# Kernel optimization log

Measured on AMD Instinct MI355X. Metric: run time of the kernel, lower is better.

## Reference

```python
import math
import jax, jax.numpy as jnp
import numpy as np

T, B, C, H = 1024, 4, 1024, 16
D = C // H  # d_k = 64


def setup_inputs() -> dict:
    key = jax.random.key(0)
    ks = jax.random.split(key, 16)
    s = 0.02
    return {
        "query": jax.random.normal(ks[0], (T, B, C), jnp.float32),
        "key": jax.random.normal(ks[1], (T, B, C), jnp.float32),
        "value": jax.random.normal(ks[2], (T, B, C), jnp.float32),
        "pos_emb": jax.random.normal(ks[3], (2 * T - 1, 1, C), jnp.float32),
        "Wq": jax.random.normal(ks[4], (C, C), jnp.float32) * s,
        "bq": jnp.zeros((C,), jnp.float32),
        "Wk": jax.random.normal(ks[5], (C, C), jnp.float32) * s,
        "bk": jnp.zeros((C,), jnp.float32),
        "Wv": jax.random.normal(ks[6], (C, C), jnp.float32) * s,
        "bv": jnp.zeros((C,), jnp.float32),
        "Wp": jax.random.normal(ks[7], (C, C), jnp.float32) * s,
        "Wo": jax.random.normal(ks[8], (C, C), jnp.float32) * s,
        "bo": jnp.zeros((C,), jnp.float32),
        "pos_bias_u": jax.random.normal(ks[9], (H, D), jnp.float32) * s,
        "pos_bias_v": jax.random.normal(ks[10], (H, D), jnp.float32) * s,
    }


def rel_shift(x):
    # x: [B, H, T, P] with P = 2T-1 -> [B, H, T, T]
    b, h, t, p = x.shape
    x = jnp.pad(x, ((0, 0), (0, 0), (0, 0), (1, 0)))  # [B,H,T,P+1]
    x = x.reshape(b, h, p + 1, t)[:, :, 1:, :].reshape(b, h, t, p)
    return x[..., : p // 2 + 1]


def reference(query, key, value, pos_emb, Wq, bq, Wk, bk, Wv, bv, Wp, Wo, bo,
              pos_bias_u, pos_bias_v):
    # T x B x C -> B x T x C
    q_in = query.transpose(1, 0, 2)
    k_in = key.transpose(1, 0, 2)
    v_in = value.transpose(1, 0, 2)
    p_in = pos_emb.transpose(1, 0, 2)  # [1, 2T-1, C]

    q = (q_in @ Wq.T + bq).reshape(B, T, H, D)            # [B,T,H,D]
    k = (k_in @ Wk.T + bk).reshape(B, T, H, D)
    v = (v_in @ Wv.T + bv).reshape(B, T, H, D)
    p = (p_in @ Wp.T).reshape(2 * T - 1, H, D)            # [2T-1,H,D]

    # content (ac) and position (bd) scores
    matrix_ac = jnp.einsum('bthd,bshd->bhts', q + pos_bias_u, k)   # [B,H,T,T]
    matrix_bd = jnp.einsum('bthd,phd->bhtp', q + pos_bias_v, p)    # [B,H,T,2T-1]
    matrix_bd = rel_shift(matrix_bd)                               # [B,H,T,T]

    scores = (matrix_ac + matrix_bd) / math.sqrt(D)
    scores = jnp.clip(scores, -1e8, 1e8)
    attn = jax.nn.softmax(scores.astype(jnp.float32), axis=-1).astype(scores.dtype)

    x = jnp.einsum('bhts,bshd->bthd', attn, v).reshape(B, T, C)
    out = x @ Wo.T + bo
    return out.transpose(1, 0, 2)  # T x B x C
```

## Files before the change

kernel.cpp:

```cpp
#include <hip/hip_runtime.h>
#include <hip/hip_bf16.h>
#include <math.h>

#define T_SEQ 1024
#define NB 4
#define NH 16
#define DD 64
#define CC 1024

typedef __attribute__((ext_vector_type(8))) short short8;
typedef __attribute__((ext_vector_type(4))) float floatx4;
typedef __attribute__((ext_vector_type(4))) unsigned short ushort4v;

#define MFMA(a, b, c) __builtin_amdgcn_mfma_f32_16x16x32_bf16((a), (b), (c), 0, 0, 0)

__device__ inline float bf2f(unsigned short u) {
  union { unsigned int i; float f; } c; c.i = ((unsigned int)u) << 16; return c.f;
}
__device__ inline unsigned short f2bf(float x) {
  union { float f; unsigned int i; } c; c.f = x;
  unsigned int u = c.i;
  u += 0x7fff + ((u >> 16) & 1);
  return (unsigned short)(u >> 16);
}

__device__ __forceinline__ void gload_lds16(const void* g, void* l) {
  __builtin_amdgcn_global_load_lds(
      (const __attribute__((address_space(1))) unsigned int*)g,
      (__attribute__((address_space(3))) unsigned int*)l, 16, 0, 0);
}

__global__ __launch_bounds__(256) void convert_kernel(
    const float* __restrict__ q, const float* __restrict__ k,
    const float* __restrict__ v, const float* __restrict__ pe_in,
    const float* __restrict__ wq, const float* __restrict__ wk,
    const float* __restrict__ wv, const float* __restrict__ wp,
    const float* __restrict__ wo,
    unsigned short* __restrict__ qo, unsigned short* __restrict__ ko,
    unsigned short* __restrict__ vo, unsigned short* __restrict__ po,
    unsigned short* __restrict__ wqo, unsigned short* __restrict__ wko,
    unsigned short* __restrict__ wvo, unsigned short* __restrict__ wpo,
    unsigned short* __restrict__ woo)
{
  const int i = blockIdx.x * 256 + threadIdx.x;
  const float* src; unsigned short* dst; int off;
  if      (i < 524288)  { src = q;     dst = qo;  off = i; }
  else if (i < 1048576) { src = k;     dst = ko;  off = i - 524288; }
  else if (i < 1572864) { src = v;     dst = vo;  off = i - 1048576; }
  else if (i < 1834880) { src = pe_in; dst = po;  off = i - 1572864; }
  else if (i < 1965952) { src = wq;    dst = wqo; off = i - 1834880; }
  else if (i < 2097024) { src = wk;    dst = wko; off = i - 1965952; }
  else if (i < 2228096) { src = wv;    dst = wvo; off = i - 2097024; }
  else if (i < 2359168) { src = wp;    dst = wpo; off = i - 2228096; }
  else if (i < 2490240) { src = wo;    dst = woo; off = i - 2359168; }
  else {
    const int j = i - 2490240;
    *(short8*)&po[2047 * 1024 + j * 8] = (short8){0, 0, 0, 0, 0, 0, 0, 0};
    return;
  }
  const float4 a0 = *(const float4*)(src + (size_t)off * 8);
  const float4 a1 = *(const float4*)(src + (size_t)off * 8 + 4);
  short8 val = (short8){(short)f2bf(a0.x), (short)f2bf(a0.y), (short)f2bf(a0.z), (short)f2bf(a0.w),
                        (short)f2bf(a1.x), (short)f2bf(a1.y), (short)f2bf(a1.z), (short)f2bf(a1.w)};
  *(short8*)&dst[(size_t)off * 8] = val;
}

template <int OUT_BF16>
__device__ __forceinline__ void gemm_core(
    const unsigned short* __restrict__ A, const unsigned short* __restrict__ Wt,
    const float* __restrict__ bias, void* __restrict__ Cv,
    unsigned short* As, unsigned short* Bs, int N, int K, int bm, int bn)
{
  const int tid = threadIdx.x;
  const int lane = tid & 63;
  const int w = tid >> 6;
  const int l15 = lane & 15, quad = lane >> 4;
  const int rw = (w >> 1) * 64, cw = (w & 1) * 64;

  floatx4 acc[4][4];
#pragma unroll
  for (int i = 0; i < 4; ++i)
#pragma unroll
    for (int j = 0; j < 4; ++j) acc[i][j] = (floatx4){0.f, 0.f, 0.f, 0.f};

  const int lrow = lane >> 2, lcol = (lane & 3) * 8;
  const unsigned short* Ag = A + (size_t)(bm + w * 32 + lrow) * K + lcol;
  const unsigned short* Wg = Wt + (size_t)(bn + w * 32 + lrow) * K + lcol;
  unsigned short* AsW = As + w * 1024;
  unsigned short* BsW = Bs + w * 1024;

  for (int k0 = 0; k0 < K; k0 += 32) {
    gload_lds16(Ag + k0, AsW);
    gload_lds16(Ag + 16 * K + k0, AsW + 512);
    gload_lds16(Wg + k0, BsW);
    gload_lds16(Wg + 16 * K + k0, BsW + 512);
    __syncthreads();

    short8 af[4], bfr[4];
#pragma unroll
    for (int i = 0; i < 4; ++i)
      af[i] = *(short8*)&As[(rw + i * 16 + l15) * 32 + quad * 8];
#pragma unroll
    for (int j = 0; j < 4; ++j)
      bfr[j] = *(short8*)&Bs[(cw + j * 16 + l15) * 32 + quad * 8];
#pragma unroll
    for (int i = 0; i < 4; ++i)
#pragma unroll
      for (int j = 0; j < 4; ++j)
        acc[i][j] = MFMA(af[i], bfr[j], acc[i][j]);
    __syncthreads();
  }

#pragma unroll
  for (int j = 0; j < 4; ++j) {
    const int col = bn + cw + j * 16 + l15;
    const float bj = bias ? bias[col] : 0.f;
#pragma unroll
    for (int i = 0; i < 4; ++i) {
      const int row0 = bm + rw + i * 16 + quad * 4;
#pragma unroll
      for (int reg = 0; reg < 4; ++reg) {
        const float v = acc[i][j][reg] + bj;
        if (OUT_BF16)
          ((unsigned short*)Cv)[(size_t)(row0 + reg) * N + col] = f2bf(v);
        else
          ((float*)Cv)[(size_t)(row0 + reg) * N + col] = v;
      }
    }
  }
}

struct GemmJob { const unsigned short* A; const unsigned short* Wt;
                 const float* bias; unsigned short* C; int mtiles; };
struct GemmJobs { GemmJob j[3]; };

__global__ __launch_bounds__(256) void gemm_qkp(GemmJobs jobs) {
  __shared__ __align__(16) unsigned short As[128 * 32];
  __shared__ __align__(16) unsigned short Bs[128 * 32];
  GemmJob jb = jobs.j[blockIdx.z];
  if ((int)blockIdx.y >= jb.mtiles) return;
  gemm_core<1>(jb.A, jb.Wt, jb.bias, jb.C, As, Bs, 1024, 1024,
               blockIdx.y * 128, blockIdx.x * 128);
}

template <int OUT_BF16>
__global__ __launch_bounds__(256) void gemm_one(
    const unsigned short* __restrict__ A, const unsigned short* __restrict__ Wt,
    const float* __restrict__ bias, void* __restrict__ Cv) {
  __shared__ __align__(16) unsigned short As[128 * 32];
  __shared__ __align__(16) unsigned short Bs[128 * 32];
  gemm_core<OUT_BF16>(A, Wt, bias, Cv, As, Bs, 1024, 1024,
                      blockIdx.y * 128, blockIdx.x * 128);
}

__global__ __launch_bounds__(256) void transpose_v(
    const unsigned short* __restrict__ vb, unsigned short* __restrict__ vT)
{
  __shared__ __align__(16) unsigned short Lt[64 * 136];
  const int t0 = blockIdx.x * 128;
  const int h = blockIdx.y, b = blockIdx.z;
  const int tid = threadIdx.x;

#pragma unroll
  for (int cc = 0; cc < 4; ++cc) {
    const int idx = tid + cc * 256;
    const int r = idx >> 3, pc = idx & 7;
    short8 val = *(const short8*)(vb + ((size_t)((t0 + r) * 4 + b)) * 1024 + h * 64 + pc * 8);
#pragma unroll
    for (int e = 0; e < 8; ++e)
      Lt[(pc * 8 + e) * 136 + r] = (unsigned short)val[e];
  }
  __syncthreads();
#pragma unroll
  for (int cc = 0; cc < 4; ++cc) {
    const int idx = tid + cc * 256;
    const int d = idx >> 4, tc = idx & 15;
    short8 v2 = *(short8*)&Lt[d * 136 + tc * 8];
    *(short8*)(vT + ((size_t)((b * 16 + h) * 64 + d)) * 1024 + t0 + tc * 8) = v2;
  }
}

__global__ __launch_bounds__(256) void precompute_kernel(
    const unsigned short* __restrict__ kb, const unsigned short* __restrict__ pb,
    const float* __restrict__ pbu, const float* __restrict__ pbv,
    float* __restrict__ uk, float* __restrict__ vp)
{
  const int i = blockIdx.x * 256 + threadIdx.x;
  if (i < 65536) {
    const int b = i >> 14, h = (i >> 10) & 15, s = i & 1023;
    const unsigned short* kr = kb + ((size_t)(s * 4 + b)) * 1024 + h * 64;
    const float* ur = pbu + h * 64;
    float sum = 0.f;
#pragma unroll
    for (int c = 0; c < 8; ++c) {
      short8 kv = *(const short8*)(kr + c * 8);
#pragma unroll
      for (int e = 0; e < 8; ++e) sum += bf2f((unsigned short)kv[e]) * ur[c * 8 + e];
    }
    uk[i] = sum;
  } else if (i < 98304) {
    const int j = i - 65536;
    const int idx = j >> 4, h = j & 15;
    const unsigned short* pr = pb + (size_t)idx * 1024 + h * 64;
    const float* vr = pbv + h * 64;
    float sum = 0.f;
#pragma unroll
    for (int c = 0; c < 8; ++c) {
      short8 pv = *(const short8*)(pr + c * 8);
#pragma unroll
      for (int e = 0; e < 8; ++e) sum += bf2f((unsigned short)pv[e]) * vr[c * 8 + e];
    }
    vp[(idx << 4) + h] = sum;
  }
}

__global__ __launch_bounds__(256) void attn_kernel(
    const unsigned short* __restrict__ qb, const unsigned short* __restrict__ kb,
    const unsigned short* __restrict__ pb, const unsigned short* __restrict__ vT,
    const float* __restrict__ uk, const float* __restrict__ vp,
    unsigned short* __restrict__ xb)
{
  __shared__ __align__(16) unsigned short Pb[64 * 136];
  __shared__ __align__(16) float BDf[64 * 196];
  __shared__ float uk_s[128], vp_w[192];
  __shared__ float pmax[2][64], psum[2][64];
  __shared__ float m_row[64], l_row[64], alpha_row[64];

  const int tid = threadIdx.x;
  const int lane = tid & 63;
  const int w = tid >> 6;
  const int l15 = lane & 15, quad = lane >> 4;
  const int th = w & 1, sh = w >> 1;

  const int flat = blockIdx.x + (blockIdx.y << 4) + (blockIdx.z << 8);
  const int x8 = flat & 7, s8 = flat >> 3;
  const int hb = x8 * 8 + (s8 >> 4);
  const int t0 = (s8 & 15) * 64;
  const int b = hb >> 4, h = hb & 15;

  short8 qf[2][2];
#pragma unroll
  for (int tt = 0; tt < 2; ++tt)
#pragma unroll
    for (int kk = 0; kk < 2; ++kk) {
      const int t = t0 + th * 32 + tt * 16 + l15;
      qf[tt][kk] = *(const short8*)(qb + ((size_t)(t * 4 + b)) * 1024 + h * 64 + kk * 32 + quad * 8);
    }

  floatx4 of[2][2];
#pragma unroll
  for (int i = 0; i < 2; ++i)
#pragma unroll
    for (int j = 0; j < 2; ++j) of[i][j] = (floatx4){0.f, 0.f, 0.f, 0.f};

  if (tid < 64) { m_row[tid] = -3.0e38f; l_row[tid] = 0.f; }
  __syncthreads();

  for (int s0 = 0; s0 < 1024; s0 += 128) {
    const int w0 = s0 - t0 + 960;

    if (tid < 128) uk_s[tid] = uk[((b * 16 + h) << 10) + s0 + tid];
    if (tid < 192) vp_w[tid] = vp[(((size_t)(w0 + tid)) << 4) + h];

    {
      floatx4 bd[6][2];
#pragma unroll
      for (int jt = 0; jt < 6; ++jt) {
        const int jj = sh * 96 + jt * 16 + l15;
        const unsigned short* pr = pb + ((size_t)(w0 + jj)) * 1024 + h * 64;
        short8 pf0 = *(const short8*)(pr + quad * 8);
        short8 pf1 = *(const short8*)(pr + 32 + quad * 8);
#pragma unroll
        for (int tt = 0; tt < 2; ++tt) {
          floatx4 z = (floatx4){0.f, 0.f, 0.f, 0.f};
          z = MFMA(pf0, qf[tt][0], z);
          z = MFMA(pf1, qf[tt][1], z);
          bd[jt][tt] = z;
        }
      }
#pragma unroll
      for (int jt = 0; jt < 6; ++jt)
#pragma unroll
        for (int tt = 0; tt < 2; ++tt) {
          const int tloc = th * 32 + tt * 16 + l15;
          const int jjb = sh * 96 + jt * 16 + quad * 4;
          *(float4*)&BDf[tloc * 196 + jjb] =
              make_float4(bd[jt][tt][0], bd[jt][tt][1], bd[jt][tt][2], bd[jt][tt][3]);
        }
    }

    floatx4 st[4][2];
#pragma unroll
    for (int stile = 0; stile < 4; ++stile) {
      const int srow = s0 + sh * 64 + stile * 16 + l15;
      const unsigned short* kr = kb + ((size_t)(srow * 4 + b)) * 1024 + h * 64;
      short8 kf0 = *(const short8*)(kr + quad * 8);
      short8 kf1 = *(const short8*)(kr + 32 + quad * 8);
#pragma unroll
      for (int tt = 0; tt < 2; ++tt) {
        floatx4 z = (floatx4){0.f, 0.f, 0.f, 0.f};
        z = MFMA(kf0, qf[tt][0], z);
        z = MFMA(kf1, qf[tt][1], z);
        st[stile][tt] = z;
      }
    }
    __syncthreads();

    float lmax[2] = {-3.0e38f, -3.0e38f};
#pragma unroll
    for (int stile = 0; stile < 4; ++stile)
#pragma unroll
      for (int tt = 0; tt < 2; ++tt) {
        const int tloc = th * 32 + tt * 16 + l15;
#pragma unroll
        for (int reg = 0; reg < 4; ++reg) {
          const int sloc = sh * 64 + stile * 16 + quad * 4 + reg;
          const int jj = sloc - tloc + 63;
          float v = 0.125f * (st[stile][tt][reg] + BDf[tloc * 196 + jj] +
                              uk_s[sloc] + vp_w[jj]);
          st[stile][tt][reg] = v;
          lmax[tt] = fmaxf(lmax[tt], v);
        }
      }
#pragma unroll
    for (int tt = 0; tt < 2; ++tt) {
      lmax[tt] = fmaxf(lmax[tt], __shfl_xor(lmax[tt], 16));
      lmax[tt] = fmaxf(lmax[tt], __shfl_xor(lmax[tt], 32));
    }
    if (quad == 0) {
      pmax[sh][th * 32 + l15] = lmax[0];
      pmax[sh][th * 32 + 16 + l15] = lmax[1];
    }
    __syncthreads();

    if (tid < 64) {
      const float mo = m_row[tid];
      const float mn = fmaxf(mo, fmaxf(pmax[0][tid], pmax[1][tid]));
      alpha_row[tid] = __expf(mo - mn);
      m_row[tid] = mn;
    }
    __syncthreads();

    float lsum[2] = {0.f, 0.f};
    float mt[2];
#pragma unroll
    for (int tt = 0; tt < 2; ++tt) mt[tt] = m_row[th * 32 + tt * 16 + l15];
#pragma unroll
    for (int stile = 0; stile < 4; ++stile)
#pragma unroll
      for (int tt = 0; tt < 2; ++tt) {
        float p0 = __expf(st[stile][tt][0] - mt[tt]);
        float p1 = __expf(st[stile][tt][1] - mt[tt]);
        float p2 = __expf(st[stile][tt][2] - mt[tt]);
        float p3 = __expf(st[stile][tt][3] - mt[tt]);
        lsum[tt] += p0 + p1 + p2 + p3;
        const int tloc = th * 32 + tt * 16 + l15;
        const int sb = sh * 64 + stile * 16 + quad * 4;
        ushort4v pk = (ushort4v){f2bf(p0), f2bf(p1), f2bf(p2), f2bf(p3)};
        *(ushort4v*)&Pb[tloc * 136 + sb] = pk;
      }
#pragma unroll
    for (int tt = 0; tt < 2; ++tt) {
      lsum[tt] += __shfl_xor(lsum[tt], 16);
      lsum[tt] += __shfl_xor(lsum[tt], 32);
    }
    if (quad == 0) {
      psum[sh][th * 32 + l15] = lsum[0];
      psum[sh][th * 32 + 16 + l15] = lsum[1];
    }
#pragma unroll
    for (int tt = 0; tt < 2; ++tt)
#pragma unroll
      for (int reg = 0; reg < 4; ++reg) {
        const float ar = alpha_row[th * 32 + tt * 16 + quad * 4 + reg];
        of[tt][0][reg] *= ar;
        of[tt][1][reg] *= ar;
      }
    __syncthreads();

    if (tid < 64)
      l_row[tid] = l_row[tid] * alpha_row[tid] + psum[0][tid] + psum[1][tid];
#pragma unroll
    for (int kk2 = 0; kk2 < 4; ++kk2) {
      short8 pa[2], vf[2];
#pragma unroll
      for (int tt = 0; tt < 2; ++tt)
        pa[tt] = *(short8*)&Pb[(th * 32 + tt * 16 + l15) * 136 + kk2 * 32 + quad * 8];
#pragma unroll
      for (int dt = 0; dt < 2; ++dt)
        vf[dt] = *(const short8*)(vT + ((size_t)((b * 16 + h) * 64 + sh * 32 + dt * 16 + l15)) * 1024 +
                                  s0 + kk2 * 32 + quad * 8);
#pragma unroll
      for (int tt = 0; tt < 2; ++tt)
#pragma unroll
        for (int dt = 0; dt < 2; ++dt)
          of[tt][dt] = MFMA(pa[tt], vf[dt], of[tt][dt]);
    }
  }
  __syncthreads();

#pragma unroll
  for (int tt = 0; tt < 2; ++tt)
#pragma unroll
    for (int reg = 0; reg < 4; ++reg) {
      const int t = th * 32 + tt * 16 + quad * 4 + reg;
      const float il = 1.f / l_row[t];
#pragma unroll
      for (int dt = 0; dt < 2; ++dt) {
        const int d = sh * 32 + dt * 16 + l15;
        xb[((size_t)((t0 + t) * 4 + b)) * 1024 + h * 64 + d] = f2bf(of[tt][dt][reg] * il);
      }
    }
}

extern "C" void kernel_launch(void* const* d_in, const int* in_sizes, int n_in,
                              void* d_out, int out_size, void* d_ws, size_t ws_size,
                              hipStream_t stream) {
  const float* query   = (const float*)d_in[0];
  const float* key_    = (const float*)d_in[1];
  const float* value   = (const float*)d_in[2];
  const float* pos_emb = (const float*)d_in[3];
  const float* Wq  = (const float*)d_in[4];
  const float* bq  = (const float*)d_in[5];
  const float* Wk  = (const float*)d_in[6];
  const float* bk  = (const float*)d_in[7];
  const float* Wv  = (const float*)d_in[8];
  const float* bv  = (const float*)d_in[9];
  const float* Wp  = (const float*)d_in[10];
  const float* Wo  = (const float*)d_in[11];
  const float* bo  = (const float*)d_in[12];
  const float* pbu = (const float*)d_in[13];
  const float* pbv = (const float*)d_in[14];
  float* out = (float*)d_out;

  unsigned short* U = (unsigned short*)d_ws;
  unsigned short* qin = U;
  unsigned short* kin = U + 4194304;
  unsigned short* vin = U + 8388608;
  unsigned short* pe  = U + 12582912;
  unsigned short* wq  = U + 14680064;
  unsigned short* wk  = U + 15728640;
  unsigned short* wv  = U + 16777216;
  unsigned short* wp  = U + 17825792;
  unsigned short* wo  = U + 18874368;
  unsigned short* qb  = U + 19922944;
  unsigned short* kb  = U + 24117248;
  unsigned short* pb  = U + 28311552;
  unsigned short* vTb = U + 30408704;
  unsigned short* vpo = kin;
  unsigned short* xb  = qin;
  float* fbase = (float*)(U + 34603008);
  float* uk = fbase;
  float* vp = fbase + 65536;

  const dim3 blk(256);

  convert_kernel<<<dim3(9728), blk, 0, stream>>>(
      query, key_, value, pos_emb, Wq, Wk, Wv, Wp, Wo,
      qin, kin, vin, pe, wq, wk, wv, wp, wo);

  GemmJobs jobs;
  jobs.j[0] = GemmJob{qin, wq, bq, qb, 32};
  jobs.j[1] = GemmJob{kin, wk, bk, kb, 32};
  jobs.j[2] = GemmJob{pe,  wp, nullptr, pb, 16};
  gemm_qkp<<<dim3(8, 32, 3), blk, 0, stream>>>(jobs);

  gemm_one<1><<<dim3(8, 32), blk, 0, stream>>>(vin, wv, bv, vpo);

  transpose_v<<<dim3(8, 16, 4), blk, 0, stream>>>(vpo, vTb);

  precompute_kernel<<<dim3(384), blk, 0, stream>>>(kb, pb, pbu, pbv, uk, vp);

  attn_kernel<<<dim3(16, 16, 4), blk, 0, stream>>>(qb, kb, pb, vTb, uk, vp, xb);

  gemm_one<0><<<dim3(8, 32), blk, 0, stream>>>(xb, wo, bo, out);
}
```

Before: 352.8 us.

## Merge V GEMM into batched projection launch and slim attention kernel LDS/sync

Folds the V projection GEMM into the batched Q/K/P GEMM launch, saving one kernel launch and giving the GPU a larger grid. In the attention kernel the BD and P tiles now share one LDS buffer, and the running max and sum move from shared memory into registers. This removes per-iteration barriers and lets the launch bound request three blocks per CU. V fragments are also loaded at the top of each tile to hide latency. The costs are higher register pressure and aliasing the vT buffer onto the pe workspace, which must not be live when the transpose writes it.

```diff
diff --git a/kernel.cpp b/kernel.cpp
--- a/kernel.cpp
+++ b/kernel.cpp
@@ -132,9 +132,9 @@
 
 struct GemmJob { const unsigned short* A; const unsigned short* Wt;
                  const float* bias; unsigned short* C; int mtiles; };
-struct GemmJobs { GemmJob j[3]; };
-
-__global__ __launch_bounds__(256) void gemm_qkp(GemmJobs jobs) {
+struct GemmJobs { GemmJob j[4]; };
+
+__global__ __launch_bounds__(256) void gemm_qkvp(GemmJobs jobs) {
   __shared__ __align__(16) unsigned short As[128 * 32];
   __shared__ __align__(16) unsigned short Bs[128 * 32];
   GemmJob jb = jobs.j[blockIdx.z];
@@ -214,17 +214,18 @@
   }
 }
 
-__global__ __launch_bounds__(256) void attn_kernel(
+__global__ __launch_bounds__(256, 3) void attn_kernel(
     const unsigned short* __restrict__ qb, const unsigned short* __restrict__ kb,
     const unsigned short* __restrict__ pb, const unsigned short* __restrict__ vT,
     const float* __restrict__ uk, const float* __restrict__ vp,
     unsigned short* __restrict__ xb)
 {
-  __shared__ __align__(16) unsigned short Pb[64 * 136];
-  __shared__ __align__(16) float BDf[64 * 196];
+  __shared__ __align__(16) unsigned char SU[64 * 196 * 4];
+  float* BDf = (float*)SU;
+  unsigned short* Pb = (unsigned short*)SU;
   __shared__ float uk_s[128], vp_w[192];
   __shared__ float pmax[2][64], psum[2][64];
-  __shared__ float m_row[64], l_row[64], alpha_row[64];
+  __shared__ float alpha_s[64];
 
   const int tid = threadIdx.x;
   const int lane = tid & 63;
@@ -253,40 +254,38 @@
 #pragma unroll
     for (int j = 0; j < 2; ++j) of[i][j] = (floatx4){0.f, 0.f, 0.f, 0.f};
 
-  if (tid < 64) { m_row[tid] = -3.0e38f; l_row[tid] = 0.f; }
-  __syncthreads();
+  float m_reg[2] = {-3.0e38f, -3.0e38f};
+  float l_reg[2][4] = {{0.f, 0.f, 0.f, 0.f}, {0.f, 0.f, 0.f, 0.f}};
 
   for (int s0 = 0; s0 < 1024; s0 += 128) {
     const int w0 = s0 - t0 + 960;
 
+    short8 vf[4][2];
+#pragma unroll
+    for (int kk2 = 0; kk2 < 4; ++kk2)
+#pragma unroll
+      for (int dt = 0; dt < 2; ++dt)
+        vf[kk2][dt] = *(const short8*)(vT + ((size_t)((b * 16 + h) * 64 + sh * 32 + dt * 16 + l15)) * 1024 +
+                                       s0 + kk2 * 32 + quad * 8);
+
     if (tid < 128) uk_s[tid] = uk[((b * 16 + h) << 10) + s0 + tid];
     if (tid < 192) vp_w[tid] = vp[(((size_t)(w0 + tid)) << 4) + h];
 
-    {
-      floatx4 bd[6][2];
-#pragma unroll
-      for (int jt = 0; jt < 6; ++jt) {
-        const int jj = sh * 96 + jt * 16 + l15;
-        const unsigned short* pr = pb + ((size_t)(w0 + jj)) * 1024 + h * 64;
-        short8 pf0 = *(const short8*)(pr + quad * 8);
-        short8 pf1 = *(const short8*)(pr + 32 + quad * 8);
-#pragma unroll
-        for (int tt = 0; tt < 2; ++tt) {
-          floatx4 z = (floatx4){0.f, 0.f, 0.f, 0.f};
-          z = MFMA(pf0, qf[tt][0], z);
-          z = MFMA(pf1, qf[tt][1], z);
-          bd[jt][tt] = z;
-        }
-      }
-#pragma unroll
-      for (int jt = 0; jt < 6; ++jt)
-#pragma unroll
-        for (int tt = 0; tt < 2; ++tt) {
-          const int tloc = th * 32 + tt * 16 + l15;
-          const int jjb = sh * 96 + jt * 16 + quad * 4;
-          *(float4*)&BDf[tloc * 196 + jjb] =
-              make_float4(bd[jt][tt][0], bd[jt][tt][1], bd[jt][tt][2], bd[jt][tt][3]);
-        }
+#pragma unroll
+    for (int jt = 0; jt < 6; ++jt) {
+      const int jj = sh * 96 + jt * 16 + l15;
+      const unsigned short* pr = pb + ((size_t)(w0 + jj)) * 1024 + h * 64;
+      short8 pf0 = *(const short8*)(pr + quad * 8);
+      short8 pf1 = *(const short8*)(pr + 32 + quad * 8);
+#pragma unroll
+      for (int tt = 0; tt < 2; ++tt) {
+        floatx4 z = (floatx4){0.f, 0.f, 0.f, 0.f};
+        z = MFMA(pf0, qf[tt][0], z);
+        z = MFMA(pf1, qf[tt][1], z);
+        const int tloc = th * 32 + tt * 16 + l15;
+        const int jjb = sh * 96 + jt * 16 + quad * 4;
+        *(float4*)&BDf[tloc * 196 + jjb] = make_float4(z[0], z[1], z[2], z[3]);
+      }
     }
 
     floatx4 st[4][2];
@@ -333,26 +332,27 @@
     }
     __syncthreads();
 
-    if (tid < 64) {
-      const float mo = m_row[tid];
-      const float mn = fmaxf(mo, fmaxf(pmax[0][tid], pmax[1][tid]));
-      alpha_row[tid] = __expf(mo - mn);
-      m_row[tid] = mn;
-    }
-    __syncthreads();
-
+    float alpha_sc[2];
+#pragma unroll
+    for (int tt = 0; tt < 2; ++tt) {
+      const int t = th * 32 + tt * 16 + l15;
+      const float mn = fmaxf(m_reg[tt], fmaxf(pmax[0][t], pmax[1][t]));
+      alpha_sc[tt] = __expf(m_reg[tt] - mn);
+      m_reg[tt] = mn;
+    }
+    if (sh == 0 && quad == 0) {
+      alpha_s[th * 32 + l15] = alpha_sc[0];
+      alpha_s[th * 32 + 16 + l15] = alpha_sc[1];
+    }
     float lsum[2] = {0.f, 0.f};
-    float mt[2];
-#pragma unroll
-    for (int tt = 0; tt < 2; ++tt) mt[tt] = m_row[th * 32 + tt * 16 + l15];
 #pragma unroll
     for (int stile = 0; stile < 4; ++stile)
 #pragma unroll
       for (int tt = 0; tt < 2; ++tt) {
-        float p0 = __expf(st[stile][tt][0] - mt[tt]);
-        float p1 = __expf(st[stile][tt][1] - mt[tt]);
-        float p2 = __expf(st[stile][tt][2] - mt[tt]);
-        float p3 = __expf(st[stile][tt][3] - mt[tt]);
+        float p0 = __expf(st[stile][tt][0] - m_reg[tt]);
+        float p1 = __expf(st[stile][tt][1] - m_reg[tt]);
+        float p2 = __expf(st[stile][tt][2] - m_reg[tt]);
+        float p3 = __expf(st[stile][tt][3] - m_reg[tt]);
         lsum[tt] += p0 + p1 + p2 + p3;
         const int tloc = th * 32 + tt * 16 + l15;
         const int sb = sh * 64 + stile * 16 + quad * 4;
@@ -368,43 +368,39 @@
       psum[sh][th * 32 + l15] = lsum[0];
       psum[sh][th * 32 + 16 + l15] = lsum[1];
     }
+    __syncthreads();
+
 #pragma unroll
     for (int tt = 0; tt < 2; ++tt)
 #pragma unroll
       for (int reg = 0; reg < 4; ++reg) {
-        const float ar = alpha_row[th * 32 + tt * 16 + quad * 4 + reg];
+        const int t = th * 32 + tt * 16 + quad * 4 + reg;
+        const float ar = alpha_s[t];
         of[tt][0][reg] *= ar;
         of[tt][1][reg] *= ar;
-      }
-    __syncthreads();
-
-    if (tid < 64)
-      l_row[tid] = l_row[tid] * alpha_row[tid] + psum[0][tid] + psum[1][tid];
+        l_reg[tt][reg] = l_reg[tt][reg] * ar + psum[0][t] + psum[1][t];
+      }
 #pragma unroll
     for (int kk2 = 0; kk2 < 4; ++kk2) {
-      short8 pa[2], vf[2];
+      short8 pa[2];
 #pragma unroll
       for (int tt = 0; tt < 2; ++tt)
         pa[tt] = *(short8*)&Pb[(th * 32 + tt * 16 + l15) * 136 + kk2 * 32 + quad * 8];
 #pragma unroll
-      for (int dt = 0; dt < 2; ++dt)
-        vf[dt] = *(const short8*)(vT + ((size_t)((b * 16 + h) * 64 + sh * 32 + dt * 16 + l15)) * 1024 +
-                                  s0 + kk2 * 32 + quad * 8);
-#pragma unroll
       for (int tt = 0; tt < 2; ++tt)
 #pragma unroll
         for (int dt = 0; dt < 2; ++dt)
-          of[tt][dt] = MFMA(pa[tt], vf[dt], of[tt][dt]);
-    }
-  }
-  __syncthreads();
+          of[tt][dt] = MFMA(pa[tt], vf[kk2][dt], of[tt][dt]);
+    }
+    __syncthreads();
+  }
 
 #pragma unroll
   for (int tt = 0; tt < 2; ++tt)
 #pragma unroll
     for (int reg = 0; reg < 4; ++reg) {
       const int t = th * 32 + tt * 16 + quad * 4 + reg;
-      const float il = 1.f / l_row[t];
+      const float il = 1.f / l_reg[tt][reg];
 #pragma unroll
       for (int dt = 0; dt < 2; ++dt) {
         const int d = sh * 32 + dt * 16 + l15;
@@ -446,8 +442,8 @@
   unsigned short* qb  = U + 19922944;
   unsigned short* kb  = U + 24117248;
   unsigned short* pb  = U + 28311552;
-  unsigned short* vTb = U + 30408704;
-  unsigned short* vpo = kin;
+  unsigned short* vpo = U + 30408704;
+  unsigned short* vTb = pe;
   unsigned short* xb  = qin;
   float* fbase = (float*)(U + 34603008);
   float* uk = fbase;
@@ -462,10 +458,9 @@
   GemmJobs jobs;
   jobs.j[0] = GemmJob{qin, wq, bq, qb, 32};
   jobs.j[1] = GemmJob{kin, wk, bk, kb, 32};
-  jobs.j[2] = GemmJob{pe,  wp, nullptr, pb, 16};
-  gemm_qkp<<<dim3(8, 32, 3), blk, 0, stream>>>(jobs);
-
-  gemm_one<1><<<dim3(8, 32), blk, 0, stream>>>(vin, wv, bv, vpo);
+  jobs.j[2] = GemmJob{vin, wv, bv, vpo, 32};
+  jobs.j[3] = GemmJob{pe,  wp, nullptr, pb, 16};
+  gemm_qkvp<<<dim3(8, 32, 4), blk, 0, stream>>>(jobs);
 
   transpose_v<<<dim3(8, 16, 4), blk, 0, stream>>>(vpo, vTb);
 
```

Measured after the change: 375.0 us. 6.3% more time.

## Prefetch next K/P fragments in attention loop and batch V projection into grouped GEMM

Applied to the files above, without the earlier changes.

The attention kernel now loads the K and positional-projection fragments for the next 128-key block into registers while the current block's MFMAs and softmax run, so global-load latency overlaps compute. A barrier is added at the end of each loop iteration to keep the shared buffers safe. Separately, the V projection GEMM is merged into the grouped Q/K/P launch (4 jobs), and workspace buffers are remapped so the V output no longer aliases the K input. This raises register pressure in the attention kernel and adds one extra sync per iteration.

```diff
diff --git a/kernel.cpp b/kernel.cpp
--- a/kernel.cpp
+++ b/kernel.cpp
@@ -132,9 +132,9 @@
 
 struct GemmJob { const unsigned short* A; const unsigned short* Wt;
                  const float* bias; unsigned short* C; int mtiles; };
-struct GemmJobs { GemmJob j[3]; };
-
-__global__ __launch_bounds__(256) void gemm_qkp(GemmJobs jobs) {
+struct GemmJobs { GemmJob j[4]; };
+
+__global__ __launch_bounds__(256) void gemm_qkvp(GemmJobs jobs) {
   __shared__ __align__(16) unsigned short As[128 * 32];
   __shared__ __align__(16) unsigned short Bs[128 * 32];
   GemmJob jb = jobs.j[blockIdx.z];
@@ -256,52 +256,71 @@
   if (tid < 64) { m_row[tid] = -3.0e38f; l_row[tid] = 0.f; }
   __syncthreads();
 
+  const unsigned short* kbase = kb + ((size_t)((sh * 64 + l15) * 4 + b)) * 1024 + h * 64;
+  const unsigned short* pbase0 = pb + ((size_t)(sh * 96 + l15)) * 1024 + h * 64;
+
+  short8 kf[4][2], pf[6][2];
+  {
+    const int w0 = 0 - t0 + 960;
+#pragma unroll
+    for (int st4 = 0; st4 < 4; ++st4) {
+      const unsigned short* kr = kbase + (size_t)(st4 * 16) * 4096;
+      kf[st4][0] = *(const short8*)(kr + quad * 8);
+      kf[st4][1] = *(const short8*)(kr + 32 + quad * 8);
+    }
+#pragma unroll
+    for (int jt = 0; jt < 6; ++jt) {
+      const unsigned short* pr = pbase0 + (size_t)(w0 + jt * 16) * 1024;
+      pf[jt][0] = *(const short8*)(pr + quad * 8);
+      pf[jt][1] = *(const short8*)(pr + 32 + quad * 8);
+    }
+  }
+
   for (int s0 = 0; s0 < 1024; s0 += 128) {
     const int w0 = s0 - t0 + 960;
 
     if (tid < 128) uk_s[tid] = uk[((b * 16 + h) << 10) + s0 + tid];
     if (tid < 192) vp_w[tid] = vp[(((size_t)(w0 + tid)) << 4) + h];
 
-    {
-      floatx4 bd[6][2];
-#pragma unroll
-      for (int jt = 0; jt < 6; ++jt) {
-        const int jj = sh * 96 + jt * 16 + l15;
-        const unsigned short* pr = pb + ((size_t)(w0 + jj)) * 1024 + h * 64;
-        short8 pf0 = *(const short8*)(pr + quad * 8);
-        short8 pf1 = *(const short8*)(pr + 32 + quad * 8);
-#pragma unroll
-        for (int tt = 0; tt < 2; ++tt) {
-          floatx4 z = (floatx4){0.f, 0.f, 0.f, 0.f};
-          z = MFMA(pf0, qf[tt][0], z);
-          z = MFMA(pf1, qf[tt][1], z);
-          bd[jt][tt] = z;
-        }
-      }
-#pragma unroll
-      for (int jt = 0; jt < 6; ++jt)
-#pragma unroll
-        for (int tt = 0; tt < 2; ++tt) {
-          const int tloc = th * 32 + tt * 16 + l15;
-          const int jjb = sh * 96 + jt * 16 + quad * 4;
-          *(float4*)&BDf[tloc * 196 + jjb] =
-              make_float4(bd[jt][tt][0], bd[jt][tt][1], bd[jt][tt][2], bd[jt][tt][3]);
-        }
-    }
-
-    floatx4 st[4][2];
-#pragma unroll
-    for (int stile = 0; stile < 4; ++stile) {
-      const int srow = s0 + sh * 64 + stile * 16 + l15;
-      const unsigned short* kr = kb + ((size_t)(srow * 4 + b)) * 1024 + h * 64;
-      short8 kf0 = *(const short8*)(kr + quad * 8);
-      short8 kf1 = *(const short8*)(kr + 32 + quad * 8);
+#pragma unroll
+    for (int jt = 0; jt < 6; ++jt) {
 #pragma unroll
       for (int tt = 0; tt < 2; ++tt) {
         floatx4 z = (floatx4){0.f, 0.f, 0.f, 0.f};
-        z = MFMA(kf0, qf[tt][0], z);
-        z = MFMA(kf1, qf[tt][1], z);
+        z = MFMA(pf[jt][0], qf[tt][0], z);
+        z = MFMA(pf[jt][1], qf[tt][1], z);
+        const int tloc = th * 32 + tt * 16 + l15;
+        const int jjb = sh * 96 + jt * 16 + quad * 4;
+        *(float4*)&BDf[tloc * 196 + jjb] = make_float4(z[0], z[1], z[2], z[3]);
+      }
+    }
+
+    floatx4 st[4][2];
+#pragma unroll
+    for (int stile = 0; stile < 4; ++stile) {
+#pragma unroll
+      for (int tt = 0; tt < 2; ++tt) {
+        floatx4 z = (floatx4){0.f, 0.f, 0.f, 0.f};
+        z = MFMA(kf[stile][0], qf[tt][0], z);
+        z = MFMA(kf[stile][1], qf[tt][1], z);
         st[stile][tt] = z;
+      }
+    }
+
+    {
+      const int s0n = (s0 + 128 < 1024) ? (s0 + 128) : 0;
+      const int w0n = s0n - t0 + 960;
+#pragma unroll
+      for (int st4 = 0; st4 < 4; ++st4) {
+        const unsigned short* kr = kbase + (size_t)(s0n + st4 * 16) * 4096;
+        kf[st4][0] = *(const short8*)(kr + quad * 8);
+        kf[st4][1] = *(const short8*)(kr + 32 + quad * 8);
+      }
+#pragma unroll
+      for (int jt = 0; jt < 6; ++jt) {
+        const unsigned short* pr = pbase0 + (size_t)(w0n + jt * 16) * 1024;
+        pf[jt][0] = *(const short8*)(pr + quad * 8);
+        pf[jt][1] = *(const short8*)(pr + 32 + quad * 8);
       }
     }
     __syncthreads();
@@ -396,8 +415,8 @@
         for (int dt = 0; dt < 2; ++dt)
           of[tt][dt] = MFMA(pa[tt], vf[dt], of[tt][dt]);
     }
-  }
-  __syncthreads();
+    __syncthreads();
+  }
 
 #pragma unroll
   for (int tt = 0; tt < 2; ++tt)
@@ -446,8 +465,8 @@
   unsigned short* qb  = U + 19922944;
   unsigned short* kb  = U + 24117248;
   unsigned short* pb  = U + 28311552;
-  unsigned short* vTb = U + 30408704;
-  unsigned short* vpo = kin;
+  unsigned short* vpo = U + 30408704;
+  unsigned short* vTb = pe;
   unsigned short* xb  = qin;
   float* fbase = (float*)(U + 34603008);
   float* uk = fbase;
@@ -462,10 +481,9 @@
   GemmJobs jobs;
   jobs.j[0] = GemmJob{qin, wq, bq, qb, 32};
   jobs.j[1] = GemmJob{kin, wk, bk, kb, 32};
-  jobs.j[2] = GemmJob{pe,  wp, nullptr, pb, 16};
-  gemm_qkp<<<dim3(8, 32, 3), blk, 0, stream>>>(jobs);
-
-  gemm_one<1><<<dim3(8, 32), blk, 0, stream>>>(vin, wv, bv, vpo);
+  jobs.j[2] = GemmJob{vin, wv, bv, vpo, 32};
+  jobs.j[3] = GemmJob{pe,  wp, nullptr, pb, 16};
+  gemm_qkvp<<<dim3(8, 32, 4), blk, 0, stream>>>(jobs);
 
   transpose_v<<<dim3(8, 16, 4), blk, 0, stream>>>(vpo, vTb);
 
```

Result: no change. 351.2 us (-0.5%).
